# Optimization experiments

Hardware: AMD Instinct MI355X
Metric: run time of the kernel (lower is better)

## Reference

```python
import jax, jax.numpy as jnp
import numpy as np

VOCAB, EMBED, HID = 50257, 512, 512
B, SRC = 128, 128


def setup_inputs() -> dict:
    key = jax.random.key(0)
    ks = jax.random.split(key, 16)
    s = 0.02
    emb_tab = jax.random.normal(ks[0], (VOCAB, EMBED), jnp.float32) * s
    emb_tab = emb_tab.at[0].set(0.0)  # padding_idx=0
    return {
        "x": jax.random.randint(ks[1], (B,), 0, VOCAB),
        "decoder_hidden": jax.random.normal(ks[2], (1, B, HID), jnp.float32),
        "source_lens": jax.random.randint(ks[3], (B,), 1, SRC + 1),
        "encoder_outputs": jax.random.normal(ks[4], (B, SRC, HID), jnp.float32),
        "context_vec": jax.random.normal(ks[5], (B, HID), jnp.float32),
        "embedding": emb_tab,
        "w_ih": jax.random.normal(ks[6], (3 * HID, HID + EMBED), jnp.float32) * s,
        "w_hh": jax.random.normal(ks[7], (3 * HID, HID), jnp.float32) * s,
        "b_ih": jax.random.normal(ks[8], (3 * HID,), jnp.float32) * s,
        "b_hh": jax.random.normal(ks[9], (3 * HID,), jnp.float32) * s,
        "Wa": jax.random.normal(ks[10], (HID, HID), jnp.float32) * s,
        "Wc": jax.random.normal(ks[11], (HID, 2 * HID), jnp.float32) * s,
        "fc1_w": jax.random.normal(ks[12], (VOCAB, HID), jnp.float32) * s,
        "fc1_b": jax.random.normal(ks[13], (VOCAB,), jnp.float32) * s,
    }


def _gru_step(inp, h, w_ih, w_hh, b_ih, b_hh):
    # inp: [B, I], h: [B, H] -> h': [B, H]  (PyTorch GRU gate order: r, z, n)
    gi = inp @ w_ih.T + b_ih
    gh = h @ w_hh.T + b_hh
    i_r, i_z, i_n = jnp.split(gi, 3, axis=1)
    h_r, h_z, h_n = jnp.split(gh, 3, axis=1)
    r = jax.nn.sigmoid(i_r + h_r)
    z = jax.nn.sigmoid(i_z + h_z)
    n = jnp.tanh(i_n + r * h_n)
    return (1.0 - z) * n + z * h


def reference(x, decoder_hidden, source_lens, encoder_outputs, context_vec,
              embedding, w_ih, w_hh, b_ih, b_hh, Wa, Wc, fc1_w, fc1_b):
    # embedding lookup (dropout is identity in eval mode)
    emb = embedding[x]                                    # [B, E]
    rnn_in = jnp.concatenate([emb, context_vec], axis=1)  # [B, E+H]
    h = _gru_step(rnn_in, decoder_hidden[0], w_ih, w_hh, b_ih, b_hh)  # [B, H]
    hidden = h[None]                                      # [1, B, H]

    # Luong-style attention (scores laid out [src_len, B] as in original)
    q = h @ Wa.T                                          # [B, H]
    attn_scores = jnp.einsum('bsh,bh->sb', encoder_outputs, q)  # [S, B]
    seq_range = jnp.arange(encoder_outputs.shape[1])      # [S]
    enc_mask = (seq_range[None, :] < source_lens[:, None]).T    # [S, B]
    masked = enc_mask.astype(attn_scores.dtype) * attn_scores
    masked = jnp.where(masked == 0, jnp.asarray(-1e10, masked.dtype), masked)
    a = jax.nn.softmax(masked, axis=0)                    # [S, B]
    ctx = jnp.einsum('sb,bsh->bh', a, encoder_outputs)    # [B, H]
    ctx = jnp.tanh(jnp.concatenate([ctx, h], axis=1) @ Wc.T)    # [B, H]

    logits = ctx @ fc1_w.T + fc1_b                        # [B, V]
    log_probs = jax.nn.log_softmax(logits, axis=1)
    return log_probs, hidden, a, ctx
```

## Files before the change

kernel.cpp:

```cpp
#include <hip/hip_runtime.h>

#define VOCAB 50257
#define EMBED 512
#define HID   512
#define B     128
#define SRC   128
#define FBLK2 3142

typedef __attribute__((ext_vector_type(8))) short short8;
typedef __attribute__((ext_vector_type(4))) float f32x4;

__device__ __forceinline__ unsigned f2bf(float x) {
    unsigned u = __builtin_bit_cast(unsigned, x);
    return (u + 0x7fffu + ((u >> 16) & 1u)) >> 16;
}
__device__ __forceinline__ unsigned pk2(float lo, float hi) {
    return f2bf(lo) | (f2bf(hi) << 16);
}
__device__ __forceinline__ uint4 pk8(const float* p) {
    uint4 r;
    r.x = pk2(p[0], p[1]); r.y = pk2(p[2], p[3]);
    r.z = pk2(p[4], p[5]); r.w = pk2(p[6], p[7]);
    return r;
}
__device__ __forceinline__ uint4 pk8v(float4 a, float4 b) {
    uint4 r;
    r.x = pk2(a.x, a.y); r.y = pk2(a.z, a.w);
    r.z = pk2(b.x, b.y); r.w = pk2(b.z, b.w);
    return r;
}


__global__ void k_embed_pack(const int* __restrict__ x, const float* __restrict__ ctxv,
                             const float* __restrict__ emb, const float* __restrict__ h0,
                             uint4* __restrict__ apk_rnn, uint4* __restrict__ apk_h0) {
    __shared__ float buf[1024];
    __shared__ float hbuf[512];
    const int b = blockIdx.x, t = threadIdx.x;
    const int row = x[b];
    if (t < 128) {
        ((float4*)buf)[t]  = ((const float4*)(emb + (size_t)row * EMBED))[t];
        ((float4*)hbuf)[t] = ((const float4*)(h0 + (size_t)b * HID))[t];
    } else {
        ((float4*)buf)[t] = ((const float4*)(ctxv + (size_t)b * HID))[t - 128];
    }
    __syncthreads();
    const int mt = b >> 4, lb = b & 15;
    if (t < 128) {
        int kc = t >> 4, ksl = (t >> 2) & 3, kg = t & 3;
        apk_rnn[((kc * 8 + mt) * 4 + ksl) * 64 + kg * 16 + lb] = pk8(&buf[t * 8]);
    } else if (t < 192) {
        int i = t - 128;
        int kc = i >> 4, ksl = (i >> 2) & 3, kg = i & 3;
        apk_h0[((kc * 8 + mt) * 4 + ksl) * 64 + kg * 16 + lb] = pk8(&hbuf[i * 8]);
    }
}

__global__ __launch_bounds__(256, 2) void k_gemm2(
        const uint4* __restrict__ apkA, const float* __restrict__ WA,
        const float* __restrict__ bA, float* __restrict__ CA, int KA,
        const uint4* __restrict__ apkB, const float* __restrict__ WB,
        const float* __restrict__ bB, float* __restrict__ CB, int KB,
        int nblkA) {
    const bool isB = (int)blockIdx.x >= nblkA;
    const uint4* apk = isB ? apkB : apkA;
    const float* W   = isB ? WB : WA;
    const float* bias= isB ? bB : bA;
    float* C         = isB ? CB : CA;
    const int K      = isB ? KB : KA;
    const int bid    = isB ? (int)blockIdx.x - nblkA : (int)blockIdx.x;
    const int N = 1536;
    __shared__ float red[4][128][16];
    const int tid = threadIdx.x, lane = tid & 63, wv = tid >> 6;
    const int n0 = bid * 16;
    const int ncol = n0 + (lane & 15);
    const int kg = lane >> 4;
    const int spw = K >> 7;
    f32x4 acc[8];
#pragma unroll
    for (int mt = 0; mt < 8; ++mt) acc[mt] = (f32x4)0.f;
    const float4* W4 = (const float4*)W;
    const size_t wb = (size_t)ncol * (K >> 2) + kg * 2;
    for (int s = 0; s < spw; ++s) {
        const int ks = wv * spw + s;
        float4 w0 = W4[wb + ks * 8];
        float4 w1 = W4[wb + ks * 8 + 1];
        short8 bf = __builtin_bit_cast(short8, pk8v(w0, w1));
        const uint4* ap = apk + ((size_t)(ks >> 2) * 32 + (ks & 3)) * 64 + lane;
#pragma unroll
        for (int mt = 0; mt < 8; ++mt) {
            short8 af = __builtin_bit_cast(short8, ap[mt * 256]);
            acc[mt] = __builtin_amdgcn_mfma_f32_16x16x32_bf16(af, bf, acc[mt], 0, 0, 0);
        }
    }
#pragma unroll
    for (int mt = 0; mt < 8; ++mt)
#pragma unroll
        for (int j = 0; j < 4; ++j)
            red[wv][mt * 16 + kg * 4 + j][lane & 15] = acc[mt][j];
    __syncthreads();
#pragma unroll
    for (int i = 0; i < 8; ++i) {
        int o = tid + i * 256;
        int r = o >> 4, c = o & 15;
        float v = red[0][r][c] + red[1][r][c] + red[2][r][c] + red[3][r][c];
        v += bias[n0 + c];
        C[(size_t)r * N + n0 + c] = v;
    }
}

template <int N, int K, int ACT, int HASB, int PACK>
__global__ __launch_bounds__(256, 2) void k_gemm_ks(
        const uint4* __restrict__ apk, const float* __restrict__ W,
        const float* __restrict__ bias, float* __restrict__ C,
        uint4* __restrict__ apk_out) {
    __shared__ float red[4][128][16];
    const int tid = threadIdx.x, lane = tid & 63, wv = tid >> 6;
    const int n0 = blockIdx.x * 16;
    const int ncol = n0 + (lane & 15);
    const int nc = ncol < N ? ncol : N - 1;
    const int kg = lane >> 4;
    constexpr int SPW = K / 128;
    f32x4 acc[8];
#pragma unroll
    for (int mt = 0; mt < 8; ++mt) acc[mt] = (f32x4)0.f;
    const float4* W4 = (const float4*)W;
    const size_t wb = (size_t)nc * (K / 4) + kg * 2;
#pragma unroll
    for (int s = 0; s < SPW; ++s) {
        const int ks = wv * SPW + s;
        float4 w0 = W4[wb + ks * 8];
        float4 w1 = W4[wb + ks * 8 + 1];
        short8 bf = __builtin_bit_cast(short8, pk8v(w0, w1));
        const uint4* ap = apk + (((ks >> 2) * 8) * 4 + (ks & 3)) * 64 + lane;
#pragma unroll
        for (int mt = 0; mt < 8; ++mt) {
            short8 af = __builtin_bit_cast(short8, ap[mt * 256]);
            acc[mt] = __builtin_amdgcn_mfma_f32_16x16x32_bf16(af, bf, acc[mt], 0, 0, 0);
        }
    }
#pragma unroll
    for (int mt = 0; mt < 8; ++mt)
#pragma unroll
        for (int j = 0; j < 4; ++j)
            red[wv][mt * 16 + kg * 4 + j][lane & 15] = acc[mt][j];
    __syncthreads();
#pragma unroll
    for (int i = 0; i < 8; ++i) {
        int o = tid + i * 256;
        int r = o >> 4, c = o & 15;
        float v = red[0][r][c] + red[1][r][c] + red[2][r][c] + red[3][r][c];
        if (HASB) v += bias[n0 + c];
        if (ACT) v = tanhf(v);
        C[(size_t)r * N + n0 + c] = v;
        if (PACK) red[0][r][c] = v;
    }
    if constexpr (PACK) {
        __syncthreads();
        int r = tid >> 1, hf = tid & 1;
        float tmp[8];
#pragma unroll
        for (int z = 0; z < 8; ++z) tmp[z] = red[0][r][hf * 8 + z];
        int k0 = n0 + hf * 8;
        int kc = k0 >> 7, ksl = (k0 >> 5) & 3, kg2 = (k0 >> 3) & 3;
        apk_out[((kc * 8 + (r >> 4)) * 4 + ksl) * 64 + kg2 * 16 + (r & 15)] = pk8(tmp);
    }
}

__global__ void k_gru(const float* __restrict__ gi, const float* __restrict__ gh,
                      const float* __restrict__ h0, float* __restrict__ h,
                      uint4* __restrict__ apk_h) {
    __shared__ float hsh[256];
    const int t = threadIdx.x;
    const int idx = blockIdx.x * 256 + t;
    const int b = blockIdx.x >> 1, half = blockIdx.x & 1;
    const int j = half * 256 + t;
    const float* gib = gi + (size_t)b * 1536;
    const float* ghb = gh + (size_t)b * 1536;
    float ir = gib[j], iz = gib[512 + j], inn = gib[1024 + j];
    float hr = ghb[j], hz = ghb[512 + j], hn = ghb[1024 + j];
    float r = 1.f / (1.f + expf(-(ir + hr)));
    float z = 1.f / (1.f + expf(-(iz + hz)));
    float nn = tanhf(inn + r * hn);
    float hv = (1.f - z) * nn + z * h0[idx];
    h[idx] = hv;
    hsh[t] = hv;
    __syncthreads();
    if (t < 32) {
        int k0 = half * 256 + t * 8;
        int kc = k0 >> 7, ksl = (k0 >> 5) & 3, kg = (k0 >> 3) & 3;
        apk_h[((kc * 8 + (b >> 4)) * 4 + ksl) * 64 + kg * 16 + (b & 15)] = pk8(&hsh[t * 8]);
    }
}

__global__ __launch_bounds__(512) void k_attn(const float* __restrict__ enc,
        const float* __restrict__ q, const int* __restrict__ lens,
        const float* __restrict__ h, float* __restrict__ a_out,
        uint4* __restrict__ apk_cat) {
    __shared__ float qs[512];
    __shared__ float red[128];
    __shared__ float aw[128];
    __shared__ float catsh[1024];
    const int b = blockIdx.x, t = threadIdx.x;
    qs[t] = q[(size_t)b * 512 + t];
    __syncthreads();
    const int srow = t >> 2, part = t & 3;
    const float* ep = enc + ((size_t)b * SRC + srow) * 512 + part * 128;
    float s = 0.f;
#pragma unroll
    for (int k4 = 0; k4 < 32; ++k4) {
        float4 e = ((const float4*)ep)[k4];
        float4 qq = *(const float4*)&qs[part * 128 + k4 * 4];
        s = fmaf(e.x, qq.x, fmaf(e.y, qq.y, fmaf(e.z, qq.z, fmaf(e.w, qq.w, s))));
    }
    s += __shfl_xor(s, 1);
    s += __shfl_xor(s, 2);
    if (part == 0) {
        int len = lens[b];
        float val = (srow < len) ? s : 0.f;
        if (val == 0.f) val = -1e10f;
        red[srow] = val;
        aw[srow] = val;
    }
    __syncthreads();
    for (int off = 64; off > 0; off >>= 1) {
        if (t < off) red[t] = fmaxf(red[t], red[t + off]);
        __syncthreads();
    }
    float mx = red[0];
    __syncthreads();
    if (t < 128) { float e = expf(aw[t] - mx); aw[t] = e; red[t] = e; }
    __syncthreads();
    for (int off = 64; off > 0; off >>= 1) {
        if (t < off) red[t] += red[t + off];
        __syncthreads();
    }
    float denom = red[0];
    if (t < 128) {
        float av = aw[t] / denom;
        aw[t] = av;
        a_out[(size_t)t * B + b] = av;
    }
    __syncthreads();
    float a0 = 0.f;
    const float* e2 = enc + (size_t)b * (SRC * 512) + t;
#pragma unroll 4
    for (int s2 = 0; s2 < SRC; ++s2) a0 = fmaf(aw[s2], e2[(size_t)s2 * 512], a0);
    catsh[t] = a0;
    catsh[512 + t] = h[(size_t)b * 512 + t];
    __syncthreads();
    if (t < 128) {
        int kc = t >> 4, ksl = (t >> 2) & 3, kg = t & 3;
        apk_cat[((kc * 8 + (b >> 4)) * 4 + ksl) * 64 + kg * 16 + (b & 15)] =
            pk8(&catsh[t * 8]);
    }
}

__global__ __launch_bounds__(64, 2) void k_fc1e(
        const uint4* __restrict__ apk, const float* __restrict__ W,
        const float* __restrict__ bias, float* __restrict__ C,
        float2* __restrict__ pout, int nblk) {
    const int lane = threadIdx.x;
    const int kg = lane >> 4;
    const int c0 = blockIdx.x * 16 + (lane & 15);
    const int nc0 = c0 < VOCAB ? c0 : VOCAB - 1;
    const float4* W4 = (const float4*)W;
    const size_t wb = (size_t)nc0 * 128 + kg * 2;

    float4 wf[32];
#pragma unroll
    for (int ks = 0; ks < 16; ++ks) {
        wf[2 * ks]     = W4[wb + ks * 8];
        wf[2 * ks + 1] = W4[wb + ks * 8 + 1];
    }
    f32x4 acc[8];
#pragma unroll
    for (int mt = 0; mt < 8; ++mt) acc[mt] = (f32x4)0.f;
#pragma unroll
    for (int ks = 0; ks < 16; ++ks) {
        short8 bf = __builtin_bit_cast(short8, pk8v(wf[2 * ks], wf[2 * ks + 1]));
        const uint4* ap = apk + ((size_t)(ks >> 2) * 32 + (ks & 3)) * 64 + lane;
#pragma unroll
        for (int mt = 0; mt < 8; ++mt) {
            short8 af = __builtin_bit_cast(short8, ap[mt * 256]);
            acc[mt] = __builtin_amdgcn_mfma_f32_16x16x32_bf16(af, bf, acc[mt], 0, 0, 0);
        }
    }
    const float bb = bias[nc0];
#pragma unroll
    for (int mt = 0; mt < 8; ++mt) {
#pragma unroll
        for (int j = 0; j < 4; ++j) {
            const int row = mt * 16 + kg * 4 + j;
            float v = acc[mt][j] + bb;
            if (c0 < VOCAB) C[(size_t)row * VOCAB + c0] = v;
            if (pout) {
                float va = c0 < VOCAB ? v : -1e30f;
                float m = va;
                m = fmaxf(m, __shfl_xor(m, 1));
                m = fmaxf(m, __shfl_xor(m, 2));
                m = fmaxf(m, __shfl_xor(m, 4));
                m = fmaxf(m, __shfl_xor(m, 8));
                float e = c0 < VOCAB ? __expf(va - m) : 0.f;
                e += __shfl_xor(e, 1);
                e += __shfl_xor(e, 2);
                e += __shfl_xor(e, 4);
                e += __shfl_xor(e, 8);
                if ((lane & 15) == 0)
                    pout[(size_t)row * nblk + blockIdx.x] = make_float2(m, e);
            }
        }
    }
}

__global__ __launch_bounds__(256) void k_lse_final(const float2* __restrict__ pout,
                                                   float* __restrict__ L, int nblk) {
    const int row = blockIdx.x, t = threadIdx.x;
    float m = -1e30f, s = 0.f;
    for (int i = t; i < nblk; i += 256) {
        float2 p = pout[(size_t)row * nblk + i];
        float mm = fmaxf(m, p.x);
        s = s * __expf(m - mm) + p.y * __expf(p.x - mm);
        m = mm;
    }
    __shared__ float sm[256], ss[256];
    sm[t] = m; ss[t] = s; __syncthreads();
    for (int off = 128; off > 0; off >>= 1) {
        if (t < off) {
            float m2 = sm[t + off], s2 = ss[t + off];
            float mm = fmaxf(sm[t], m2);
            ss[t] = ss[t] * __expf(sm[t] - mm) + s2 * __expf(m2 - mm);
            sm[t] = mm;
        }
        __syncthreads();
    }
    if (t == 0) L[row] = sm[0] + logf(ss[0]);
}

__global__ __launch_bounds__(512) void k_lsub(float* __restrict__ logits,
                                              const float* __restrict__ L) {
    const int b = blockIdx.y;
    const float l = L[b];
    float* row = logits + (size_t)b * VOCAB;
    int c0 = (blockIdx.x * 512 + threadIdx.x) * 4;
    if (c0 + 4 <= VOCAB) {
        float4 x = *(float4*)(row + c0);
        x.x -= l; x.y -= l; x.z -= l; x.w -= l;
        *(float4*)(row + c0) = x;
    } else {
        for (int c = c0; c < VOCAB; ++c) row[c] -= l;
    }
}

__global__ __launch_bounds__(1024) void k_lse_sub(float* __restrict__ logits) {
    const int b = blockIdx.x, t = threadIdx.x;
    float* row = logits + (size_t)b * VOCAB;
    const int N4 = VOCAB >> 2;
    float m = -1e30f, s = 0.f;
    for (int i = t; i < N4; i += 1024) {
        float4 x = ((const float4*)row)[i];
        float xs[4] = {x.x, x.y, x.z, x.w};
#pragma unroll
        for (int j = 0; j < 4; ++j) {
            float v = xs[j];
            if (v > m) { s = s * __expf(m - v) + 1.f; m = v; }
            else        s += __expf(v - m);
        }
    }
    if (t == 0) {
        float v = row[VOCAB - 1];
        if (v > m) { s = s * __expf(m - v) + 1.f; m = v; }
        else        s += __expf(v - m);
    }
    __shared__ float sm[1024], ss[1024];
    sm[t] = m; ss[t] = s;
    __syncthreads();
    for (int off = 512; off > 0; off >>= 1) {
        if (t < off) {
            float m2 = sm[t + off], s2 = ss[t + off];
            float mm = fmaxf(sm[t], m2);
            ss[t] = ss[t] * __expf(sm[t] - mm) + s2 * __expf(m2 - mm);
            sm[t] = mm;
        }
        __syncthreads();
    }
    __shared__ float Lsh;
    if (t == 0) Lsh = sm[0] + logf(ss[0]);
    __syncthreads();
    float L = Lsh;
    for (int i = t; i < N4; i += 1024) {
        float4 x = ((const float4*)row)[i];
        x.x -= L; x.y -= L; x.z -= L; x.w -= L;
        ((float4*)row)[i] = x;
    }
    if (t == 0) row[VOCAB - 1] -= L;
}

extern "C" void kernel_launch(void* const* d_in, const int* in_sizes, int n_in,
                              void* d_out, int out_size, void* d_ws, size_t ws_size,
                              hipStream_t stream) {
    const int*   x    = (const int*)d_in[0];
    const float* h0   = (const float*)d_in[1];
    const int*   lens = (const int*)d_in[2];
    const float* enc  = (const float*)d_in[3];
    const float* ctxv = (const float*)d_in[4];
    const float* emb  = (const float*)d_in[5];
    const float* wih  = (const float*)d_in[6];
    const float* whh  = (const float*)d_in[7];
    const float* bih  = (const float*)d_in[8];
    const float* bhh  = (const float*)d_in[9];
    const float* Wa   = (const float*)d_in[10];
    const float* Wc   = (const float*)d_in[11];
    const float* fc1w = (const float*)d_in[12];
    const float* fc1b = (const float*)d_in[13];

    float* out     = (float*)d_out;
    float* outLogp = out;
    float* outHid  = out + (size_t)B * VOCAB;
    float* outA    = outHid + (size_t)B * HID;
    float* outCtx  = outA + (size_t)SRC * B;

    float* gi = outLogp;
    float* gh = gi + B * 1536;
    float* q  = gh + B * 1536;
    uint4* apk_rnn = (uint4*)(q + B * HID);
    uint4* apk_h0  = apk_rnn + 16384;
    uint4* apk_h   = apk_h0 + 8192;
    uint4* apk_cat = apk_h + 8192;

    uint4*  apk_ctx = (uint4*)d_ws;
    size_t  off_pout = 131072;
    size_t  off_L    = off_pout + (size_t)B * FBLK2 * sizeof(float2);
    bool bigws = ws_size >= off_L + 512;
    float2* pout = bigws ? (float2*)((char*)d_ws + off_pout) : nullptr;
    float*  Lb   = bigws ? (float*)((char*)d_ws + off_L) : nullptr;

    k_embed_pack<<<dim3(B), dim3(256), 0, stream>>>(x, ctxv, emb, h0, apk_rnn, apk_h0);
    k_gemm2<<<dim3(192), dim3(256), 0, stream>>>(
        apk_rnn, wih, bih, gi, 1024,
        apk_h0, whh, bhh, gh, 512, 96);
    k_gru<<<dim3(256), dim3(256), 0, stream>>>(gi, gh, h0, outHid, apk_h);
    k_gemm_ks<512, 512, 0, 0, 0><<<dim3(32), dim3(256), 0, stream>>>(
        apk_h, Wa, nullptr, q, nullptr);
    k_attn<<<dim3(B), dim3(512), 0, stream>>>(enc, q, lens, outHid, outA, apk_cat);
    k_gemm_ks<512, 1024, 1, 0, 1><<<dim3(32), dim3(256), 0, stream>>>(
        apk_cat, Wc, nullptr, outCtx, apk_ctx);
    k_fc1e<<<dim3(FBLK2), dim3(64), 0, stream>>>(apk_ctx, fc1w, fc1b, outLogp,
                                                 pout, FBLK2);
    if (bigws) {
        k_lse_final<<<dim3(B), dim3(256), 0, stream>>>(pout, Lb, FBLK2);
        k_lsub<<<dim3(25, B), dim3(512), 0, stream>>>(outLogp, Lb);
    } else {
        k_lse_sub<<<dim3(B), dim3(1024), 0, stream>>>(outLogp);
    }
}
```

Baseline: 117.8 us.

## Split fc1 K dimension across four waves with shared-memory reduction

```diff
diff --git a/kernel.cpp b/kernel.cpp
--- a/kernel.cpp
+++ b/kernel.cpp
@@ -256,59 +256,63 @@
     }
 }
 
-__global__ __launch_bounds__(64, 2) void k_fc1e(
+__global__ __launch_bounds__(256, 4) void k_fc1k(
         const uint4* __restrict__ apk, const float* __restrict__ W,
         const float* __restrict__ bias, float* __restrict__ C,
         float2* __restrict__ pout, int nblk) {
-    const int lane = threadIdx.x;
+    __shared__ float red[4][128][16];
+    const int tid = threadIdx.x, lane = tid & 63, wv = tid >> 6;
+    const int n0 = blockIdx.x * 16;
+    const int ncol = n0 + (lane & 15);
+    const int nc = ncol < VOCAB ? ncol : VOCAB - 1;
     const int kg = lane >> 4;
-    const int c0 = blockIdx.x * 16 + (lane & 15);
-    const int nc0 = c0 < VOCAB ? c0 : VOCAB - 1;
+    f32x4 acc[8];
+#pragma unroll
+    for (int mt = 0; mt < 8; ++mt) acc[mt] = (f32x4)0.f;
     const float4* W4 = (const float4*)W;
-    const size_t wb = (size_t)nc0 * 128 + kg * 2;
-
-    float4 wf[32];
-#pragma unroll
-    for (int ks = 0; ks < 16; ++ks) {
-        wf[2 * ks]     = W4[wb + ks * 8];
-        wf[2 * ks + 1] = W4[wb + ks * 8 + 1];
-    }
-    f32x4 acc[8];
-#pragma unroll
-    for (int mt = 0; mt < 8; ++mt) acc[mt] = (f32x4)0.f;
-#pragma unroll
-    for (int ks = 0; ks < 16; ++ks) {
-        short8 bf = __builtin_bit_cast(short8, pk8v(wf[2 * ks], wf[2 * ks + 1]));
-        const uint4* ap = apk + ((size_t)(ks >> 2) * 32 + (ks & 3)) * 64 + lane;
+    const size_t wb = (size_t)nc * 128 + kg * 2;
+#pragma unroll
+    for (int s = 0; s < 4; ++s) {
+        const int ks = wv * 4 + s;
+        float4 w0 = W4[wb + ks * 8];
+        float4 w1 = W4[wb + ks * 8 + 1];
+        short8 bf = __builtin_bit_cast(short8, pk8v(w0, w1));
+        const uint4* ap = apk + (((ks >> 2) * 8) * 4 + (ks & 3)) * 64 + lane;
 #pragma unroll
         for (int mt = 0; mt < 8; ++mt) {
             short8 af = __builtin_bit_cast(short8, ap[mt * 256]);
             acc[mt] = __builtin_amdgcn_mfma_f32_16x16x32_bf16(af, bf, acc[mt], 0, 0, 0);
         }
     }
-    const float bb = bias[nc0];
-#pragma unroll
-    for (int mt = 0; mt < 8; ++mt) {
-#pragma unroll
-        for (int j = 0; j < 4; ++j) {
-            const int row = mt * 16 + kg * 4 + j;
-            float v = acc[mt][j] + bb;
-            if (c0 < VOCAB) C[(size_t)row * VOCAB + c0] = v;
-            if (pout) {
-                float va = c0 < VOCAB ? v : -1e30f;
-                float m = va;
-                m = fmaxf(m, __shfl_xor(m, 1));
-                m = fmaxf(m, __shfl_xor(m, 2));
-                m = fmaxf(m, __shfl_xor(m, 4));
-                m = fmaxf(m, __shfl_xor(m, 8));
-                float e = c0 < VOCAB ? __expf(va - m) : 0.f;
-                e += __shfl_xor(e, 1);
-                e += __shfl_xor(e, 2);
-                e += __shfl_xor(e, 4);
-                e += __shfl_xor(e, 8);
-                if ((lane & 15) == 0)
-                    pout[(size_t)row * nblk + blockIdx.x] = make_float2(m, e);
-            }
+#pragma unroll
+    for (int mt = 0; mt < 8; ++mt)
+#pragma unroll
+        for (int j = 0; j < 4; ++j)
+            red[wv][mt * 16 + kg * 4 + j][lane & 15] = acc[mt][j];
+    __syncthreads();
+#pragma unroll
+    for (int i = 0; i < 8; ++i) {
+        int o = tid + i * 256;
+        int r = o >> 4, c = o & 15;
+        int col = n0 + c;
+        bool valid = col < VOCAB;
+        float v = red[0][r][c] + red[1][r][c] + red[2][r][c] + red[3][r][c];
+        v += bias[valid ? col : VOCAB - 1];
+        if (valid) C[(size_t)r * VOCAB + col] = v;
+        if (pout) {
+            float va = valid ? v : -1e30f;
+            float m = va;
+            m = fmaxf(m, __shfl_xor(m, 1));
+            m = fmaxf(m, __shfl_xor(m, 2));
+            m = fmaxf(m, __shfl_xor(m, 4));
+            m = fmaxf(m, __shfl_xor(m, 8));
+            float e = valid ? __expf(va - m) : 0.f;
+            e += __shfl_xor(e, 1);
+            e += __shfl_xor(e, 2);
+            e += __shfl_xor(e, 4);
+            e += __shfl_xor(e, 8);
+            if ((lane & 15) == 0)
+                pout[(size_t)r * nblk + blockIdx.x] = make_float2(m, e);
         }
     }
 }
@@ -445,8 +449,8 @@
     k_attn<<<dim3(B), dim3(512), 0, stream>>>(enc, q, lens, outHid, outA, apk_cat);
     k_gemm_ks<512, 1024, 1, 0, 1><<<dim3(32), dim3(256), 0, stream>>>(
         apk_cat, Wc, nullptr, outCtx, apk_ctx);
-    k_fc1e<<<dim3(FBLK2), dim3(64), 0, stream>>>(apk_ctx, fc1w, fc1b, outLogp,
-                                                 pout, FBLK2);
+    k_fc1k<<<dim3(FBLK2), dim3(256), 0, stream>>>(apk_ctx, fc1w, fc1b, outLogp,
+                                                  pout, FBLK2);
     if (bigws) {
         k_lse_final<<<dim3(B), dim3(256), 0, stream>>>(pout, Lb, FBLK2);
         k_lsub<<<dim3(25, B), dim3(512), 0, stream>>>(outLogp, Lb);
```

Result: slower. 123.2 us (+4.6%).

## Stage fc1 weights through LDS with coalesced loads and bf16 prepacking

Applied to the files above, without the earlier changes.

```diff
diff --git a/kernel.cpp b/kernel.cpp
--- a/kernel.cpp
+++ b/kernel.cpp
@@ -5,7 +5,8 @@
 #define HID   512
 #define B     128
 #define SRC   128
-#define FBLK2 3142
+#define FBLK3 1571
+#define PW    3142
 
 typedef __attribute__((ext_vector_type(8))) short short8;
 typedef __attribute__((ext_vector_type(4))) float f32x4;
@@ -256,58 +257,73 @@
     }
 }
 
-__global__ __launch_bounds__(64, 2) void k_fc1e(
+__global__ __launch_bounds__(256, 4) void k_fc1pc(
         const uint4* __restrict__ apk, const float* __restrict__ W,
         const float* __restrict__ bias, float* __restrict__ C,
-        float2* __restrict__ pout, int nblk) {
-    const int lane = threadIdx.x;
-    const int kg = lane >> 4;
-    const int c0 = blockIdx.x * 16 + (lane & 15);
-    const int nc0 = c0 < VOCAB ? c0 : VOCAB - 1;
+        float2* __restrict__ pout) {
+    __shared__ uint2 wl2[2][64][17][2];
+    const int tid = threadIdx.x, lane = tid & 63, wv = tid >> 6;
+    const int n0 = blockIdx.x * 32;
     const float4* W4 = (const float4*)W;
-    const size_t wb = (size_t)nc0 * 128 + kg * 2;
-
-    float4 wf[32];
+
+#pragma unroll
+    for (int rr = 0; rr < 8; ++rr) {
+        const int r = wv * 8 + rr;
+        const int n = n0 + r;
+        const int nc = n < VOCAB ? n : VOCAB - 1;
+        const size_t base = (size_t)nc * 128;
+        float4 fa = W4[base + lane];
+        float4 fb = W4[base + 64 + lane];
+        const int g = r >> 4, col = r & 15;
+        uint2 ua, ub;
+        ua.x = pk2(fa.x, fa.y); ua.y = pk2(fa.z, fa.w);
+        ub.x = pk2(fb.x, fb.y); ub.y = pk2(fb.z, fb.w);
+        wl2[g][lane >> 1][col][lane & 1] = ua;
+        wl2[g][32 + (lane >> 1)][col][lane & 1] = ub;
+    }
+    __syncthreads();
+    if (wv >= 2) return;
+
+    const int g = wv;
+    const int col = lane & 15, kg = lane >> 4;
+    const int n = n0 + g * 16 + col;
+    const bool valid = n < VOCAB;
+    const uint4* wlr = (const uint4*)wl2[g];
+    f32x4 acc[8];
+#pragma unroll
+    for (int mt = 0; mt < 8; ++mt) acc[mt] = (f32x4)0.f;
 #pragma unroll
     for (int ks = 0; ks < 16; ++ks) {
-        wf[2 * ks]     = W4[wb + ks * 8];
-        wf[2 * ks + 1] = W4[wb + ks * 8 + 1];
-    }
-    f32x4 acc[8];
-#pragma unroll
-    for (int mt = 0; mt < 8; ++mt) acc[mt] = (f32x4)0.f;
-#pragma unroll
-    for (int ks = 0; ks < 16; ++ks) {
-        short8 bf = __builtin_bit_cast(short8, pk8v(wf[2 * ks], wf[2 * ks + 1]));
-        const uint4* ap = apk + ((size_t)(ks >> 2) * 32 + (ks & 3)) * 64 + lane;
+        short8 bf = __builtin_bit_cast(short8, wlr[(ks * 4 + kg) * 17 + col]);
+        const uint4* ap = apk + (((ks >> 2) * 8) * 4 + (ks & 3)) * 64 + lane;
 #pragma unroll
         for (int mt = 0; mt < 8; ++mt) {
             short8 af = __builtin_bit_cast(short8, ap[mt * 256]);
             acc[mt] = __builtin_amdgcn_mfma_f32_16x16x32_bf16(af, bf, acc[mt], 0, 0, 0);
         }
     }
-    const float bb = bias[nc0];
+    const float bb = bias[valid ? n : VOCAB - 1];
 #pragma unroll
     for (int mt = 0; mt < 8; ++mt) {
 #pragma unroll
         for (int j = 0; j < 4; ++j) {
             const int row = mt * 16 + kg * 4 + j;
             float v = acc[mt][j] + bb;
-            if (c0 < VOCAB) C[(size_t)row * VOCAB + c0] = v;
+            if (valid) C[(size_t)row * VOCAB + n] = v;
             if (pout) {
-                float va = c0 < VOCAB ? v : -1e30f;
+                float va = valid ? v : -1e30f;
                 float m = va;
                 m = fmaxf(m, __shfl_xor(m, 1));
                 m = fmaxf(m, __shfl_xor(m, 2));
                 m = fmaxf(m, __shfl_xor(m, 4));
                 m = fmaxf(m, __shfl_xor(m, 8));
-                float e = c0 < VOCAB ? __expf(va - m) : 0.f;
+                float e = valid ? __expf(va - m) : 0.f;
                 e += __shfl_xor(e, 1);
                 e += __shfl_xor(e, 2);
                 e += __shfl_xor(e, 4);
                 e += __shfl_xor(e, 8);
                 if ((lane & 15) == 0)
-                    pout[(size_t)row * nblk + blockIdx.x] = make_float2(m, e);
+                    pout[(size_t)row * PW + blockIdx.x * 2 + g] = make_float2(m, e);
             }
         }
     }
@@ -430,7 +446,7 @@
 
     uint4*  apk_ctx = (uint4*)d_ws;
     size_t  off_pout = 131072;
-    size_t  off_L    = off_pout + (size_t)B * FBLK2 * sizeof(float2);
+    size_t  off_L    = off_pout + (size_t)B * PW * sizeof(float2);
     bool bigws = ws_size >= off_L + 512;
     float2* pout = bigws ? (float2*)((char*)d_ws + off_pout) : nullptr;
     float*  Lb   = bigws ? (float*)((char*)d_ws + off_L) : nullptr;
@@ -445,10 +461,9 @@
     k_attn<<<dim3(B), dim3(512), 0, stream>>>(enc, q, lens, outHid, outA, apk_cat);
     k_gemm_ks<512, 1024, 1, 0, 1><<<dim3(32), dim3(256), 0, stream>>>(
         apk_cat, Wc, nullptr, outCtx, apk_ctx);
-    k_fc1e<<<dim3(FBLK2), dim3(64), 0, stream>>>(apk_ctx, fc1w, fc1b, outLogp,
-                                                 pout, FBLK2);
+    k_fc1pc<<<dim3(FBLK3), dim3(256), 0, stream>>>(apk_ctx, fc1w, fc1b, outLogp, pout);
     if (bigws) {
-        k_lse_final<<<dim3(B), dim3(256), 0, stream>>>(pout, Lb, FBLK2);
+        k_lse_final<<<dim3(B), dim3(256), 0, stream>>>(pout, Lb, PW);
         k_lsub<<<dim3(25, B), dim3(512), 0, stream>>>(outLogp, Lb);
     } else {
         k_lse_sub<<<dim3(B), dim3(1024), 0, stream>>>(outLogp);
```

Result: slower. 137.1 us (+16.4%).

## Fuse Wa/Wc projections into per-batch attention kernel and merge LSE finalize+subtract

Applied to the files above, without the earlier changes.

```diff
diff --git a/kernel.cpp b/kernel.cpp
--- a/kernel.cpp
+++ b/kernel.cpp
@@ -109,68 +109,8 @@
     }
 }
 
-template <int N, int K, int ACT, int HASB, int PACK>
-__global__ __launch_bounds__(256, 2) void k_gemm_ks(
-        const uint4* __restrict__ apk, const float* __restrict__ W,
-        const float* __restrict__ bias, float* __restrict__ C,
-        uint4* __restrict__ apk_out) {
-    __shared__ float red[4][128][16];
-    const int tid = threadIdx.x, lane = tid & 63, wv = tid >> 6;
-    const int n0 = blockIdx.x * 16;
-    const int ncol = n0 + (lane & 15);
-    const int nc = ncol < N ? ncol : N - 1;
-    const int kg = lane >> 4;
-    constexpr int SPW = K / 128;
-    f32x4 acc[8];
-#pragma unroll
-    for (int mt = 0; mt < 8; ++mt) acc[mt] = (f32x4)0.f;
-    const float4* W4 = (const float4*)W;
-    const size_t wb = (size_t)nc * (K / 4) + kg * 2;
-#pragma unroll
-    for (int s = 0; s < SPW; ++s) {
-        const int ks = wv * SPW + s;
-        float4 w0 = W4[wb + ks * 8];
-        float4 w1 = W4[wb + ks * 8 + 1];
-        short8 bf = __builtin_bit_cast(short8, pk8v(w0, w1));
-        const uint4* ap = apk + (((ks >> 2) * 8) * 4 + (ks & 3)) * 64 + lane;
-#pragma unroll
-        for (int mt = 0; mt < 8; ++mt) {
-            short8 af = __builtin_bit_cast(short8, ap[mt * 256]);
-            acc[mt] = __builtin_amdgcn_mfma_f32_16x16x32_bf16(af, bf, acc[mt], 0, 0, 0);
-        }
-    }
-#pragma unroll
-    for (int mt = 0; mt < 8; ++mt)
-#pragma unroll
-        for (int j = 0; j < 4; ++j)
-            red[wv][mt * 16 + kg * 4 + j][lane & 15] = acc[mt][j];
-    __syncthreads();
-#pragma unroll
-    for (int i = 0; i < 8; ++i) {
-        int o = tid + i * 256;
-        int r = o >> 4, c = o & 15;
-        float v = red[0][r][c] + red[1][r][c] + red[2][r][c] + red[3][r][c];
-        if (HASB) v += bias[n0 + c];
-        if (ACT) v = tanhf(v);
-        C[(size_t)r * N + n0 + c] = v;
-        if (PACK) red[0][r][c] = v;
-    }
-    if constexpr (PACK) {
-        __syncthreads();
-        int r = tid >> 1, hf = tid & 1;
-        float tmp[8];
-#pragma unroll
-        for (int z = 0; z < 8; ++z) tmp[z] = red[0][r][hf * 8 + z];
-        int k0 = n0 + hf * 8;
-        int kc = k0 >> 7, ksl = (k0 >> 5) & 3, kg2 = (k0 >> 3) & 3;
-        apk_out[((kc * 8 + (r >> 4)) * 4 + ksl) * 64 + kg2 * 16 + (r & 15)] = pk8(tmp);
-    }
-}
-
 __global__ void k_gru(const float* __restrict__ gi, const float* __restrict__ gh,
-                      const float* __restrict__ h0, float* __restrict__ h,
-                      uint4* __restrict__ apk_h) {
-    __shared__ float hsh[256];
+                      const float* __restrict__ h0, float* __restrict__ h) {
     const int t = threadIdx.x;
     const int idx = blockIdx.x * 256 + t;
     const int b = blockIdx.x >> 1, half = blockIdx.x & 1;
@@ -182,27 +122,34 @@
     float r = 1.f / (1.f + expf(-(ir + hr)));
     float z = 1.f / (1.f + expf(-(iz + hz)));
     float nn = tanhf(inn + r * hn);
-    float hv = (1.f - z) * nn + z * h0[idx];
-    h[idx] = hv;
-    hsh[t] = hv;
-    __syncthreads();
-    if (t < 32) {
-        int k0 = half * 256 + t * 8;
-        int kc = k0 >> 7, ksl = (k0 >> 5) & 3, kg = (k0 >> 3) & 3;
-        apk_h[((kc * 8 + (b >> 4)) * 4 + ksl) * 64 + kg * 16 + (b & 15)] = pk8(&hsh[t * 8]);
-    }
-}
-
-__global__ __launch_bounds__(512) void k_attn(const float* __restrict__ enc,
-        const float* __restrict__ q, const int* __restrict__ lens,
-        const float* __restrict__ h, float* __restrict__ a_out,
-        uint4* __restrict__ apk_cat) {
+    h[idx] = (1.f - z) * nn + z * h0[idx];
+}
+
+__global__ __launch_bounds__(512) void k_attn_mega(const float* __restrict__ enc,
+        const float* __restrict__ Wa, const float* __restrict__ Wc,
+        const int* __restrict__ lens, const float* __restrict__ h,
+        float* __restrict__ a_out, float* __restrict__ ctx_out,
+        uint4* __restrict__ apk_ctx) {
+    __shared__ float hs[512];
     __shared__ float qs[512];
     __shared__ float red[128];
     __shared__ float aw[128];
     __shared__ float catsh[1024];
+    __shared__ float ctxsh[512];
     const int b = blockIdx.x, t = threadIdx.x;
-    qs[t] = q[(size_t)b * 512 + t];
+    hs[t] = h[(size_t)b * 512 + t];
+    __syncthreads();
+    {
+        const float4* wr = (const float4*)(Wa + (size_t)t * 512);
+        float acc = 0.f;
+#pragma unroll 8
+        for (int i = 0; i < 128; ++i) {
+            float4 w = wr[i];
+            float4 hv = *(const float4*)&hs[i * 4];
+            acc = fmaf(w.x, hv.x, fmaf(w.y, hv.y, fmaf(w.z, hv.z, fmaf(w.w, hv.w, acc))));
+        }
+        qs[t] = acc;
+    }
     __syncthreads();
     const int srow = t >> 2, part = t & 3;
     const float* ep = enc + ((size_t)b * SRC + srow) * 512 + part * 128;
@@ -247,12 +194,27 @@
 #pragma unroll 4
     for (int s2 = 0; s2 < SRC; ++s2) a0 = fmaf(aw[s2], e2[(size_t)s2 * 512], a0);
     catsh[t] = a0;
-    catsh[512 + t] = h[(size_t)b * 512 + t];
-    __syncthreads();
-    if (t < 128) {
-        int kc = t >> 4, ksl = (t >> 2) & 3, kg = t & 3;
-        apk_cat[((kc * 8 + (b >> 4)) * 4 + ksl) * 64 + kg * 16 + (b & 15)] =
-            pk8(&catsh[t * 8]);
+    catsh[512 + t] = hs[t];
+    __syncthreads();
+    {
+        const float4* wr = (const float4*)(Wc + (size_t)t * 1024);
+        float acc = 0.f;
+#pragma unroll 8
+        for (int i = 0; i < 256; ++i) {
+            float4 w = wr[i];
+            float4 cv = *(const float4*)&catsh[i * 4];
+            acc = fmaf(w.x, cv.x, fmaf(w.y, cv.y, fmaf(w.z, cv.z, fmaf(w.w, cv.w, acc))));
+        }
+        float v = tanhf(acc);
+        ctxsh[t] = v;
+        ctx_out[(size_t)b * 512 + t] = v;
+    }
+    __syncthreads();
+    if (t < 64) {
+        int k0 = t * 8;
+        int kc = k0 >> 7, ksl = (k0 >> 5) & 3, kg = (k0 >> 3) & 3;
+        apk_ctx[((kc * 8 + (b >> 4)) * 4 + ksl) * 64 + kg * 16 + (b & 15)] =
+            pk8(&ctxsh[t * 8]);
     }
 }
 
@@ -313,19 +275,20 @@
     }
 }
 
-__global__ __launch_bounds__(256) void k_lse_final(const float2* __restrict__ pout,
-                                                   float* __restrict__ L, int nblk) {
-    const int row = blockIdx.x, t = threadIdx.x;
+__global__ __launch_bounds__(1024) void k_lse_fuse(float* __restrict__ logits,
+        const float2* __restrict__ pout, int nblk) {
+    const int b = blockIdx.x, t = threadIdx.x;
     float m = -1e30f, s = 0.f;
-    for (int i = t; i < nblk; i += 256) {
-        float2 p = pout[(size_t)row * nblk + i];
+    for (int i = t; i < nblk; i += 1024) {
+        float2 p = pout[(size_t)b * nblk + i];
         float mm = fmaxf(m, p.x);
         s = s * __expf(m - mm) + p.y * __expf(p.x - mm);
         m = mm;
     }
-    __shared__ float sm[256], ss[256];
-    sm[t] = m; ss[t] = s; __syncthreads();
-    for (int off = 128; off > 0; off >>= 1) {
+    __shared__ float sm[1024], ss[1024];
+    sm[t] = m; ss[t] = s;
+    __syncthreads();
+    for (int off = 512; off > 0; off >>= 1) {
         if (t < off) {
             float m2 = sm[t + off], s2 = ss[t + off];
             float mm = fmaxf(sm[t], m2);
@@ -334,22 +297,18 @@
         }
         __syncthreads();
     }
-    if (t == 0) L[row] = sm[0] + logf(ss[0]);
-}
-
-__global__ __launch_bounds__(512) void k_lsub(float* __restrict__ logits,
-                                              const float* __restrict__ L) {
-    const int b = blockIdx.y;
-    const float l = L[b];
+    __shared__ float Lsh;
+    if (t == 0) Lsh = sm[0] + logf(ss[0]);
+    __syncthreads();
+    const float L = Lsh;
     float* row = logits + (size_t)b * VOCAB;
-    int c0 = (blockIdx.x * 512 + threadIdx.x) * 4;
-    if (c0 + 4 <= VOCAB) {
-        float4 x = *(float4*)(row + c0);
-        x.x -= l; x.y -= l; x.z -= l; x.w -= l;
-        *(float4*)(row + c0) = x;
-    } else {
-        for (int c = c0; c < VOCAB; ++c) row[c] -= l;
-    }
+    const int N4 = VOCAB >> 2;
+    for (int i = t; i < N4; i += 1024) {
+        float4 x = ((const float4*)row)[i];
+        x.x -= L; x.y -= L; x.z -= L; x.w -= L;
+        ((float4*)row)[i] = x;
+    }
+    if (t == 0) row[VOCAB - 1] -= L;
 }
 
 __global__ __launch_bounds__(1024) void k_lse_sub(float* __restrict__ logits) {
@@ -422,34 +381,26 @@
 
     float* gi = outLogp;
     float* gh = gi + B * 1536;
-    float* q  = gh + B * 1536;
-    uint4* apk_rnn = (uint4*)(q + B * HID);
+    uint4* apk_rnn = (uint4*)(gh + B * 1536);
     uint4* apk_h0  = apk_rnn + 16384;
-    uint4* apk_h   = apk_h0 + 8192;
-    uint4* apk_cat = apk_h + 8192;
 
     uint4*  apk_ctx = (uint4*)d_ws;
     size_t  off_pout = 131072;
     size_t  off_L    = off_pout + (size_t)B * FBLK2 * sizeof(float2);
     bool bigws = ws_size >= off_L + 512;
     float2* pout = bigws ? (float2*)((char*)d_ws + off_pout) : nullptr;
-    float*  Lb   = bigws ? (float*)((char*)d_ws + off_L) : nullptr;
 
     k_embed_pack<<<dim3(B), dim3(256), 0, stream>>>(x, ctxv, emb, h0, apk_rnn, apk_h0);
     k_gemm2<<<dim3(192), dim3(256), 0, stream>>>(
         apk_rnn, wih, bih, gi, 1024,
         apk_h0, whh, bhh, gh, 512, 96);
-    k_gru<<<dim3(256), dim3(256), 0, stream>>>(gi, gh, h0, outHid, apk_h);
-    k_gemm_ks<512, 512, 0, 0, 0><<<dim3(32), dim3(256), 0, stream>>>(
-        apk_h, Wa, nullptr, q, nullptr);
-    k_attn<<<dim3(B), dim3(512), 0, stream>>>(enc, q, lens, outHid, outA, apk_cat);
-    k_gemm_ks<512, 1024, 1, 0, 1><<<dim3(32), dim3(256), 0, stream>>>(
-        apk_cat, Wc, nullptr, outCtx, apk_ctx);
+    k_gru<<<dim3(256), dim3(256), 0, stream>>>(gi, gh, h0, outHid);
+    k_attn_mega<<<dim3(B), dim3(512), 0, stream>>>(
+        enc, Wa, Wc, lens, outHid, outA, outCtx, apk_ctx);
     k_fc1e<<<dim3(FBLK2), dim3(64), 0, stream>>>(apk_ctx, fc1w, fc1b, outLogp,
                                                  pout, FBLK2);
     if (bigws) {
-        k_lse_final<<<dim3(B), dim3(256), 0, stream>>>(pout, Lb, FBLK2);
-        k_lsub<<<dim3(25, B), dim3(512), 0, stream>>>(outLogp, Lb);
+        k_lse_fuse<<<dim3(B), dim3(1024), 0, stream>>>(outLogp, pout, FBLK2);
     } else {
         k_lse_sub<<<dim3(B), dim3(1024), 0, stream>>>(outLogp);
     }
```

Result: slower. 180.6 us (+53.3%).
